# Optimization experiments

Measured on AMD Instinct MI355X. Metric: run time of the kernel, lower is better.

## Reference

```python
import jax, jax.numpy as jnp
import numpy as np
from jax.scipy.linalg import expm

B, D = 4096, 128


def setup_inputs() -> dict:
    key = jax.random.key(0)
    k1, k2, k3, k4 = jax.random.split(key, 4)
    # xavier_uniform bound for a (D, D) weight: sqrt(6 / (D + D))
    a_w = float(np.sqrt(6.0 / (D + D)))
    # xavier_uniform bound for bias of shape (1, D): sqrt(6 / (1 + D))
    a_b = float(np.sqrt(6.0 / (1 + D)))
    x = jax.random.normal(k1, (B, D), dtype=jnp.float32)
    t = jax.random.uniform(k2, (B, 1), dtype=jnp.float32)  # per-sample scalar time
    weight = jax.random.uniform(k3, (D, D), dtype=jnp.float32, minval=-a_w, maxval=a_w)
    bias = jax.random.uniform(k4, (1, D), dtype=jnp.float32, minval=-a_b, maxval=a_b)
    return {"x": x, "t": t, "weight": weight, "bias": bias}


def reference(x, t, weight, bias):
    # t: [B, 1] -> broadcast scalar per sample; A: [B, D, D]
    A = weight[None, :, :] * t[:, :, None]
    E = jax.vmap(expm)(A)                       # batched matrix exponential
    y = jnp.einsum('bij,bj->bi', E, x)          # [B, D]
    y = y + bias * t                            # bias * t.squeeze(-1)
    ljd = jnp.diagonal(weight)[None, :] * t     # diag(weight * t): [B, D]
    return (y, ljd)
```

## Files before the change

### kernel.cpp

```cpp
#include <hip/hip_runtime.h>


#define DD 128
#define KT 12
#define KS 136

typedef float    f32x4 __attribute__((ext_vector_type(4)));
typedef _Float16 f16x8 __attribute__((ext_vector_type(8)));
typedef _Float16 f16x4 __attribute__((ext_vector_type(4)));

__global__ __launch_bounds__(64, 1)
void affine_exp_kernel(const float* __restrict__ x,
                       const float* __restrict__ t,
                       const float* __restrict__ weight,
                       const float* __restrict__ bias,
                       float* __restrict__ out, int B)
{
    __shared__ _Float16 vbuf[16 * KS];

    const int l  = threadIdx.x;
    const int n  = l & 15;
    const int q  = l >> 4;
    const int s0 = blockIdx.x * 16;

    const float tn = t[s0 + n];

    f16x8 wf[8][4];
#pragma unroll
    for (int r = 0; r < 8; ++r)
#pragma unroll
        for (int kf = 0; kf < 4; ++kf) {
            const float* p = weight + (size_t)(16 * r + n) * DD + 32 * kf + 8 * q;
            const f32x4 a = *reinterpret_cast<const f32x4*>(p);
            const f32x4 b = *reinterpret_cast<const f32x4*>(p + 4);
            f16x8 h;
#pragma unroll
            for (int j = 0; j < 4; ++j) {
                h[j]     = (_Float16)a[j];
                h[j + 4] = (_Float16)b[j];
            }
            wf[r][kf] = h;
        }

    f16x8 vraw[4];
    {
        const float* xp = x + (size_t)(s0 + n) * DD + 8 * q;
#pragma unroll
        for (int kf = 0; kf < 4; ++kf) {
            const f32x4 a = *reinterpret_cast<const f32x4*>(xp + 32 * kf);
            const f32x4 b = *reinterpret_cast<const f32x4*>(xp + 32 * kf + 4);
            f16x8 h;
#pragma unroll
            for (int j = 0; j < 4; ++j) {
                h[j]     = (_Float16)a[j];
                h[j + 4] = (_Float16)b[j];
            }
            vraw[kf] = h;
        }
    }

    f32x4 y[8];
#pragma unroll
    for (int r = 0; r < 8; ++r)
        y[r] = *reinterpret_cast<const f32x4*>(x + (size_t)(s0 + n) * DD + 16 * r + 4 * q);

#pragma unroll
    for (int k = 1; k <= KT; ++k) {
        const float c = tn * (1.0f / (float)k);
        const _Float16 ch = (_Float16)c;
        f16x8 cv;
#pragma unroll
        for (int j = 0; j < 8; ++j) cv[j] = ch;

        f16x8 vb[4];
#pragma unroll
        for (int kf = 0; kf < 4; ++kf) vb[kf] = vraw[kf] * cv;

        f32x4 acc[8];
#pragma unroll
        for (int r = 0; r < 8; ++r) acc[r] = (f32x4){0.f, 0.f, 0.f, 0.f};

#pragma unroll
        for (int kf = 0; kf < 4; ++kf)
#pragma unroll
            for (int r = 0; r < 8; ++r)
                acc[r] = __builtin_amdgcn_mfma_f32_16x16x32_f16(wf[r][kf], vb[kf], acc[r], 0, 0, 0);

#pragma unroll
        for (int r = 0; r < 8; ++r) y[r] += acc[r];

        if (k < KT) {
#pragma unroll
            for (int r = 0; r < 8; ++r) {
                f16x4 pk;
#pragma unroll
                for (int jr = 0; jr < 4; ++jr) pk[jr] = (_Float16)acc[r][jr];
                *reinterpret_cast<f16x4*>(&vbuf[n * KS + 16 * r + 4 * q]) = pk;
            }
            __syncthreads();
#pragma unroll
            for (int kf = 0; kf < 4; ++kf)
                vraw[kf] = *reinterpret_cast<const f16x8*>(&vbuf[n * KS + 32 * kf + 8 * q]);
        }
    }

#pragma unroll
    for (int r = 0; r < 8; ++r) {
        const f32x4 bv = *reinterpret_cast<const f32x4*>(bias + 16 * r + 4 * q);
        const f32x4 o  = y[r] + bv * tn;
        *reinterpret_cast<f32x4*>(out + (size_t)(s0 + n) * DD + 16 * r + 4 * q) = o;
    }

    {
        const float d0 = weight[(size_t)(2 * l) * DD + 2 * l];
        const float d1 = weight[(size_t)(2 * l + 1) * DD + 2 * l + 1];
        float* lout = out + (size_t)B * DD;
#pragma unroll
        for (int j = 0; j < 16; ++j) {
            const float tj = t[s0 + j];
            *reinterpret_cast<float2*>(lout + (size_t)(s0 + j) * DD + 2 * l) =
                make_float2(d0 * tj, d1 * tj);
        }
    }
}

extern "C" void kernel_launch(void* const* d_in, const int* in_sizes, int n_in,
                              void* d_out, int out_size, void* d_ws, size_t ws_size,
                              hipStream_t stream) {
    const float* x      = (const float*)d_in[0];
    const float* t      = (const float*)d_in[1];
    const float* weight = (const float*)d_in[2];
    const float* bias   = (const float*)d_in[3];
    float* out = (float*)d_out;

    const int B = in_sizes[1];
    const int blocks = B / 16;

    affine_exp_kernel<<<blocks, 64, 0, stream>>>(x, t, weight, bias, out, B);
}
```

Measured before the change: 82.07 us.

## Restructure Taylor loop: scale after MFMA, swizzled LDS layout, no unroll

Moves the per-term scale by t/k from the f16 input vector to the f32 MFMA output, so the stored term is pre-scaled in higher precision. It replaces the padded row-major LDS buffer with a fragment-ordered layout, so each lane reads its operand as one contiguous 16-byte chunk at l*8. The Taylor loop is no longer unrolled and the MFMAs are split into two groups of four accumulators to reduce register pressure. The cost is loop overhead and less scheduling freedom across iterations, plus possible LDS bank conflicts on the scattered writes.

```diff
diff --git a/kernel.cpp b/kernel.cpp
--- a/kernel.cpp
+++ b/kernel.cpp
@@ -3,7 +3,6 @@
 
 #define DD 128
 #define KT 12
-#define KS 136
 
 typedef float    f32x4 __attribute__((ext_vector_type(4)));
 typedef _Float16 f16x8 __attribute__((ext_vector_type(8)));
@@ -16,7 +15,7 @@
                        const float* __restrict__ bias,
                        float* __restrict__ out, int B)
 {
-    __shared__ _Float16 vbuf[16 * KS];
+    __shared__ _Float16 vbuf[4 * 512];
 
     const int l  = threadIdx.x;
     const int n  = l & 15;
@@ -43,64 +42,59 @@
         }
 
     f16x8 vraw[4];
-    {
-        const float* xp = x + (size_t)(s0 + n) * DD + 8 * q;
+    const float* xp = x + (size_t)(s0 + n) * DD;
 #pragma unroll
-        for (int kf = 0; kf < 4; ++kf) {
-            const f32x4 a = *reinterpret_cast<const f32x4*>(xp + 32 * kf);
-            const f32x4 b = *reinterpret_cast<const f32x4*>(xp + 32 * kf + 4);
-            f16x8 h;
+    for (int kf = 0; kf < 4; ++kf) {
+        const f32x4 a = *reinterpret_cast<const f32x4*>(xp + 32 * kf + 8 * q);
+        const f32x4 b = *reinterpret_cast<const f32x4*>(xp + 32 * kf + 8 * q + 4);
+        f16x8 h;
 #pragma unroll
-            for (int j = 0; j < 4; ++j) {
-                h[j]     = (_Float16)a[j];
-                h[j + 4] = (_Float16)b[j];
-            }
-            vraw[kf] = h;
+        for (int j = 0; j < 4; ++j) {
+            h[j]     = (_Float16)a[j];
+            h[j + 4] = (_Float16)b[j];
         }
+        vraw[kf] = h;
     }
 
     f32x4 y[8];
 #pragma unroll
     for (int r = 0; r < 8; ++r)
-        y[r] = *reinterpret_cast<const f32x4*>(x + (size_t)(s0 + n) * DD + 16 * r + 4 * q);
+        y[r] = *reinterpret_cast<const f32x4*>(xp + 16 * r + 4 * q);
 
-#pragma unroll
+#pragma unroll 1
     for (int k = 1; k <= KT; ++k) {
         const float c = tn * (1.0f / (float)k);
-        const _Float16 ch = (_Float16)c;
-        f16x8 cv;
 #pragma unroll
-        for (int j = 0; j < 8; ++j) cv[j] = ch;
-
-        f16x8 vb[4];
+        for (int g = 0; g < 2; ++g) {
+            f32x4 acc[4];
 #pragma unroll
-        for (int kf = 0; kf < 4; ++kf) vb[kf] = vraw[kf] * cv;
-
-        f32x4 acc[8];
+            for (int rr = 0; rr < 4; ++rr) acc[rr] = (f32x4){0.f, 0.f, 0.f, 0.f};
 #pragma unroll
-        for (int r = 0; r < 8; ++r) acc[r] = (f32x4){0.f, 0.f, 0.f, 0.f};
-
+            for (int kf = 0; kf < 4; ++kf)
 #pragma unroll
-        for (int kf = 0; kf < 4; ++kf)
+                for (int rr = 0; rr < 4; ++rr)
+                    acc[rr] = __builtin_amdgcn_mfma_f32_16x16x32_f16(
+                        wf[g * 4 + rr][kf], vraw[kf], acc[rr], 0, 0, 0);
 #pragma unroll
-            for (int r = 0; r < 8; ++r)
-                acc[r] = __builtin_amdgcn_mfma_f32_16x16x32_f16(wf[r][kf], vb[kf], acc[r], 0, 0, 0);
-
+            for (int rr = 0; rr < 4; ++rr) {
+                const int r = g * 4 + rr;
+                const f32x4 vk = acc[rr] * c;
+                y[r] += vk;
+                if (k < KT) {
+                    f16x4 pk;
 #pragma unroll
-        for (int r = 0; r < 8; ++r) y[r] += acc[r];
-
+                    for (int jr = 0; jr < 4; ++jr) pk[jr] = (_Float16)vk[jr];
+                    const int kd0  = 16 * r + 4 * q;
+                    const int addr = (kd0 >> 5) * 512 + (n + 16 * ((kd0 & 31) >> 3)) * 8 + (kd0 & 7);
+                    *reinterpret_cast<f16x4*>(&vbuf[addr]) = pk;
+                }
+            }
+        }
         if (k < KT) {
-#pragma unroll
-            for (int r = 0; r < 8; ++r) {
-                f16x4 pk;
-#pragma unroll
-                for (int jr = 0; jr < 4; ++jr) pk[jr] = (_Float16)acc[r][jr];
-                *reinterpret_cast<f16x4*>(&vbuf[n * KS + 16 * r + 4 * q]) = pk;
-            }
             __syncthreads();
 #pragma unroll
             for (int kf = 0; kf < 4; ++kf)
-                vraw[kf] = *reinterpret_cast<const f16x8*>(&vbuf[n * KS + 32 * kf + 8 * q]);
+                vraw[kf] = *reinterpret_cast<const f16x8*>(&vbuf[kf * 512 + l * 8]);
         }
     }
 
```

After: 69.65 us. 1.18x faster.

## Precompute scaled weight powers W^k/k! once and apply per-sample with t^k

Applied to the files above, without the earlier changes.

Because A = t*W, the Taylor series of exp(tW)x is rewritten as sum_k t^k (W^k/k!) x. A small pre-kernel computes the scaled powers of W once in fp16 and stores them in workspace, and the apply kernel streams these matrices and accumulates t^k-scaled MFMA products. This removes the serial per-step LDS round-trip and barrier chain of the per-sample recurrence. The apply kernel splits the terms across two waves that are reduced through LDS, and the series is truncated at 10 terms instead of 12. In exchange it adds a second launch, reads the power matrices from global memory in every block, and risks fp16 accuracy loss from large t^k and W^k/k! values.

```diff
diff --git a/kernel.cpp b/kernel.cpp
--- a/kernel.cpp
+++ b/kernel.cpp
@@ -2,124 +2,170 @@
 
 
 #define DD 128
-#define KT 12
-#define KS 136
+#define KT 10
 
 typedef float    f32x4 __attribute__((ext_vector_type(4)));
 typedef _Float16 f16x8 __attribute__((ext_vector_type(8)));
-typedef _Float16 f16x4 __attribute__((ext_vector_type(4)));
 
-__global__ __launch_bounds__(64, 1)
-void affine_exp_kernel(const float* __restrict__ x,
-                       const float* __restrict__ t,
-                       const float* __restrict__ weight,
-                       const float* __restrict__ bias,
-                       float* __restrict__ out, int B)
+
+__global__ __launch_bounds__(256, 1)
+void gpow_kernel(const float* __restrict__ weight, _Float16* __restrict__ gws)
 {
-    __shared__ _Float16 vbuf[16 * KS];
+    __shared__ float wlds[DD * DD];
+    __shared__ float gbuf[2][16 * 136];
 
-    const int l  = threadIdx.x;
-    const int n  = l & 15;
-    const int q  = l >> 4;
+    const int tid = threadIdx.x;
+    const int w = tid >> 6, l = tid & 63, n = l & 15, q = l >> 4;
+    const int r = blockIdx.x;
+
+    for (int i = tid; i < DD * DD / 4; i += 256)
+        reinterpret_cast<f32x4*>(wlds)[i] = reinterpret_cast<const f32x4*>(weight)[i];
+    __syncthreads();
+
+    f16x8 Bf[2][4];
+#pragma unroll
+    for (int nt = 0; nt < 2; ++nt)
+#pragma unroll
+        for (int kf = 0; kf < 4; ++kf)
+#pragma unroll
+            for (int j = 0; j < 8; ++j)
+                Bf[nt][kf][j] = (_Float16)wlds[(32 * kf + 8 * q + j) * DD + 32 * w + 16 * nt + n];
+
+    f16x8 Af[4];
+#pragma unroll
+    for (int kf = 0; kf < 4; ++kf) {
+        const float* p = wlds + (size_t)(16 * r + n) * DD + 32 * kf + 8 * q;
+#pragma unroll
+        for (int j = 0; j < 8; ++j) Af[kf][j] = (_Float16)p[j];
+    }
+    *reinterpret_cast<f16x8*>(gws + (size_t)(((0 * 8 + r) * 4 + w)) * 512 + l * 8) = Af[w];
+
+    int cur = 0;
+#pragma unroll 1
+    for (int k = 2; k <= KT; ++k) {
+        f32x4 C0 = {0.f, 0.f, 0.f, 0.f}, C1 = {0.f, 0.f, 0.f, 0.f};
+#pragma unroll
+        for (int kf = 0; kf < 4; ++kf) {
+            C0 = __builtin_amdgcn_mfma_f32_16x16x32_f16(Af[kf], Bf[0][kf], C0, 0, 0, 0);
+            C1 = __builtin_amdgcn_mfma_f32_16x16x32_f16(Af[kf], Bf[1][kf], C1, 0, 0, 0);
+        }
+        const float inv = 1.0f / (float)k;
+        C0 *= inv;
+        C1 *= inv;
+#pragma unroll
+        for (int jr = 0; jr < 4; ++jr) {
+            gbuf[cur][(4 * q + jr) * 136 + 32 * w + n]      = C0[jr];
+            gbuf[cur][(4 * q + jr) * 136 + 32 * w + 16 + n] = C1[jr];
+        }
+        __syncthreads();
+#pragma unroll
+        for (int kf = 0; kf < 4; ++kf) {
+            const float* p = &gbuf[cur][n * 136 + 32 * kf + 8 * q];
+            const f32x4 a = *reinterpret_cast<const f32x4*>(p);
+            const f32x4 b = *reinterpret_cast<const f32x4*>(p + 4);
+#pragma unroll
+            for (int j = 0; j < 4; ++j) {
+                Af[kf][j]     = (_Float16)a[j];
+                Af[kf][j + 4] = (_Float16)b[j];
+            }
+        }
+        *reinterpret_cast<f16x8*>(gws + (size_t)((((k - 1) * 8 + r) * 4 + w)) * 512 + l * 8) = Af[w];
+        cur ^= 1;
+    }
+}
+
+__global__ __launch_bounds__(128, 1)
+void apply_kernel(const float* __restrict__ x,
+                  const float* __restrict__ t,
+                  const float* __restrict__ weight,
+                  const float* __restrict__ bias,
+                  const _Float16* __restrict__ gws,
+                  float* __restrict__ out, int B)
+{
+    __shared__ float pbuf[8 * 64 * 4];
+
+    const int tid = threadIdx.x;
+    const int h = tid >> 6, l = tid & 63, n = l & 15, q = l >> 4;
     const int s0 = blockIdx.x * 16;
 
     const float tn = t[s0 + n];
+    const float* xp = x + (size_t)(s0 + n) * DD;
 
-    f16x8 wf[8][4];
+    f16x8 xb[4];
 #pragma unroll
-    for (int r = 0; r < 8; ++r)
+    for (int kf = 0; kf < 4; ++kf) {
+        const f32x4 a = *reinterpret_cast<const f32x4*>(xp + 32 * kf + 8 * q);
+        const f32x4 b = *reinterpret_cast<const f32x4*>(xp + 32 * kf + 8 * q + 4);
 #pragma unroll
-        for (int kf = 0; kf < 4; ++kf) {
-            const float* p = weight + (size_t)(16 * r + n) * DD + 32 * kf + 8 * q;
-            const f32x4 a = *reinterpret_cast<const f32x4*>(p);
-            const f32x4 b = *reinterpret_cast<const f32x4*>(p + 4);
-            f16x8 h;
-#pragma unroll
-            for (int j = 0; j < 4; ++j) {
-                h[j]     = (_Float16)a[j];
-                h[j + 4] = (_Float16)b[j];
-            }
-            wf[r][kf] = h;
-        }
-
-    f16x8 vraw[4];
-    {
-        const float* xp = x + (size_t)(s0 + n) * DD + 8 * q;
-#pragma unroll
-        for (int kf = 0; kf < 4; ++kf) {
-            const f32x4 a = *reinterpret_cast<const f32x4*>(xp + 32 * kf);
-            const f32x4 b = *reinterpret_cast<const f32x4*>(xp + 32 * kf + 4);
-            f16x8 h;
-#pragma unroll
-            for (int j = 0; j < 4; ++j) {
-                h[j]     = (_Float16)a[j];
-                h[j + 4] = (_Float16)b[j];
-            }
-            vraw[kf] = h;
+        for (int j = 0; j < 4; ++j) {
+            xb[kf][j]     = (_Float16)a[j];
+            xb[kf][j + 4] = (_Float16)b[j];
         }
     }
 
     f32x4 y[8];
 #pragma unroll
     for (int r = 0; r < 8; ++r)
-        y[r] = *reinterpret_cast<const f32x4*>(x + (size_t)(s0 + n) * DD + 16 * r + 4 * q);
+        y[r] = (h == 0) ? *reinterpret_cast<const f32x4*>(xp + 16 * r + 4 * q)
+                        : (f32x4){0.f, 0.f, 0.f, 0.f};
 
-#pragma unroll
-    for (int k = 1; k <= KT; ++k) {
-        const float c = tn * (1.0f / (float)k);
-        const _Float16 ch = (_Float16)c;
+    float tk = tn;
+    for (int i = 0; i < 5 * h; ++i) tk *= tn;
+
+#pragma unroll 1
+    for (int kk = 0; kk < 5; ++kk) {
+        const int k = 5 * h + 1 + kk;
+        const _Float16 th = (_Float16)tk;
         f16x8 cv;
 #pragma unroll
-        for (int j = 0; j < 8; ++j) cv[j] = ch;
+        for (int j = 0; j < 8; ++j) cv[j] = th;
+        f16x8 xk[4];
+#pragma unroll
+        for (int kf = 0; kf < 4; ++kf) xk[kf] = xb[kf] * cv;
 
-        f16x8 vb[4];
+        const _Float16* gk = gws + (size_t)((k - 1) * 8) * 4 * 512 + l * 8;
+#pragma unroll 4
+        for (int r = 0; r < 8; ++r) {
+            f16x8 g0 = *reinterpret_cast<const f16x8*>(gk + (r * 4 + 0) * 512);
+            f16x8 g1 = *reinterpret_cast<const f16x8*>(gk + (r * 4 + 1) * 512);
+            f16x8 g2 = *reinterpret_cast<const f16x8*>(gk + (r * 4 + 2) * 512);
+            f16x8 g3 = *reinterpret_cast<const f16x8*>(gk + (r * 4 + 3) * 512);
+            y[r] = __builtin_amdgcn_mfma_f32_16x16x32_f16(g0, xk[0], y[r], 0, 0, 0);
+            y[r] = __builtin_amdgcn_mfma_f32_16x16x32_f16(g1, xk[1], y[r], 0, 0, 0);
+            y[r] = __builtin_amdgcn_mfma_f32_16x16x32_f16(g2, xk[2], y[r], 0, 0, 0);
+            y[r] = __builtin_amdgcn_mfma_f32_16x16x32_f16(g3, xk[3], y[r], 0, 0, 0);
+        }
+        tk *= tn;
+    }
+
+    {
+        const int s  = tid >> 3;
+        const int dg = (tid & 7) * 16;
+        const float ts = t[s0 + s];
+        float* lp = out + (size_t)B * DD + (size_t)(s0 + s) * DD + dg;
 #pragma unroll
-        for (int kf = 0; kf < 4; ++kf) vb[kf] = vraw[kf] * cv;
-
-        f32x4 acc[8];
+        for (int c = 0; c < 4; ++c) {
+            f32x4 o;
 #pragma unroll
-        for (int r = 0; r < 8; ++r) acc[r] = (f32x4){0.f, 0.f, 0.f, 0.f};
-
-#pragma unroll
-        for (int kf = 0; kf < 4; ++kf)
-#pragma unroll
-            for (int r = 0; r < 8; ++r)
-                acc[r] = __builtin_amdgcn_mfma_f32_16x16x32_f16(wf[r][kf], vb[kf], acc[r], 0, 0, 0);
-
-#pragma unroll
-        for (int r = 0; r < 8; ++r) y[r] += acc[r];
-
-        if (k < KT) {
-#pragma unroll
-            for (int r = 0; r < 8; ++r) {
-                f16x4 pk;
-#pragma unroll
-                for (int jr = 0; jr < 4; ++jr) pk[jr] = (_Float16)acc[r][jr];
-                *reinterpret_cast<f16x4*>(&vbuf[n * KS + 16 * r + 4 * q]) = pk;
-            }
-            __syncthreads();
-#pragma unroll
-            for (int kf = 0; kf < 4; ++kf)
-                vraw[kf] = *reinterpret_cast<const f16x8*>(&vbuf[n * KS + 32 * kf + 8 * q]);
+            for (int j = 0; j < 4; ++j)
+                o[j] = weight[(size_t)(dg + 4 * c + j) * DD + dg + 4 * c + j] * ts;
+            *reinterpret_cast<f32x4*>(lp + 4 * c) = o;
         }
     }
 
+    if (h == 1) {
 #pragma unroll
-    for (int r = 0; r < 8; ++r) {
-        const f32x4 bv = *reinterpret_cast<const f32x4*>(bias + 16 * r + 4 * q);
-        const f32x4 o  = y[r] + bv * tn;
-        *reinterpret_cast<f32x4*>(out + (size_t)(s0 + n) * DD + 16 * r + 4 * q) = o;
+        for (int r = 0; r < 8; ++r)
+            *reinterpret_cast<f32x4*>(&pbuf[(r * 64 + l) * 4]) = y[r];
     }
-
-    {
-        const float d0 = weight[(size_t)(2 * l) * DD + 2 * l];
-        const float d1 = weight[(size_t)(2 * l + 1) * DD + 2 * l + 1];
-        float* lout = out + (size_t)B * DD;
+    __syncthreads();
+    if (h == 0) {
 #pragma unroll
-        for (int j = 0; j < 16; ++j) {
-            const float tj = t[s0 + j];
-            *reinterpret_cast<float2*>(lout + (size_t)(s0 + j) * DD + 2 * l) =
-                make_float2(d0 * tj, d1 * tj);
+        for (int r = 0; r < 8; ++r) {
+            const f32x4 p  = *reinterpret_cast<const f32x4*>(&pbuf[(r * 64 + l) * 4]);
+            const f32x4 bv = *reinterpret_cast<const f32x4*>(bias + 16 * r + 4 * q);
+            const f32x4 o  = y[r] + p + bv * tn;
+            *reinterpret_cast<f32x4*>(out + (size_t)(s0 + n) * DD + 16 * r + 4 * q) = o;
         }
     }
 }
@@ -132,9 +178,10 @@
     const float* weight = (const float*)d_in[2];
     const float* bias   = (const float*)d_in[3];
     float* out = (float*)d_out;
+    _Float16* gws = (_Float16*)d_ws;
 
     const int B = in_sizes[1];
-    const int blocks = B / 16;
 
-    affine_exp_kernel<<<blocks, 64, 0, stream>>>(x, t, weight, bias, out, B);
+    gpow_kernel<<<8, 256, 0, stream>>>(weight, gws);
+    apply_kernel<<<B / 16, 128, 0, stream>>>(x, t, weight, bias, gws, out, B);
 }
```

Result: slower. 97.56 us (+18.9%).
